# Optimization experiments

Hardware: AMD Instinct MI355X
Metric: run time of the kernel (lower is better)

The kernel has to match this reference:

```python
import jax, jax.numpy as jnp
import numpy as np

N = 50000      # nodes
E = 800000     # edges (avg degree 16)
IN = 128       # in_feats
OUT = 128      # out_feats
H = 8          # num_heads
D = OUT // H   # out_heads (per-head dim) = 16


def _xavier(key, shape, fan_in, fan_out):
    bound = np.sqrt(6.0 / (fan_in + fan_out)).astype(np.float32)
    return jax.random.uniform(key, shape, jnp.float32, -bound, bound)


def setup_inputs() -> dict:
    key = jax.random.key(0)
    ks = jax.random.split(key, 12)
    feat = jax.random.normal(ks[0], (N, IN), jnp.float32)
    src = jax.random.randint(ks[1], (E,), 0, N, jnp.int32)
    dst = jax.random.randint(ks[2], (E,), 0, N, jnp.int32)
    # stacked per-head Linear weights: nn.Linear(IN, D) per head -> [H, IN, D]
    Wq = _xavier(ks[3], (H, IN, D), IN, D)
    Wk = _xavier(ks[4], (H, IN, D), IN, D)
    Wv = _xavier(ks[5], (H, IN, D), IN, D)
    b = 1.0 / np.sqrt(IN).astype(np.float32)
    bq = jax.random.uniform(ks[6], (H, D), jnp.float32, -b, b)
    bk = jax.random.uniform(ks[7], (H, D), jnp.float32, -b, b)
    bv = jax.random.uniform(ks[8], (H, D), jnp.float32, -b, b)
    # residual self projection W_self: Linear(IN, OUT), stored as [IN, OUT]
    Ws = _xavier(ks[9], (IN, OUT), IN, OUT)
    bs = jax.random.uniform(ks[10], (OUT,), jnp.float32, -b, b)
    return {"feat": feat, "src": src, "dst": dst,
            "Wq": Wq, "bq": bq, "Wk": Wk, "bk": bk, "Wv": Wv, "bv": bv,
            "Ws": Ws, "bs": bs}


def reference(feat, src, dst, Wq, bq, Wk, bk, Wv, bv, Ws, bs):
    # per-head projections, all heads at once: [N, H, D]
    q = jnp.einsum('ni,hid->nhd', feat, Wq) + bq
    k = jnp.einsum('ni,hid->nhd', feat, Wk) + bk
    v = jnp.einsum('ni,hid->nhd', feat, Wv) + bv

    # edge scores: sum_d k[src] * q[dst], scaled by sqrt(D)  -> [E, H]
    scores = jnp.einsum('ehd,ehd->eh', k[src], q[dst]) / np.sqrt(D).astype(np.float32)

    # edge_softmax: segment softmax over incoming edges of each dst node
    m = jax.ops.segment_max(scores, dst, num_segments=N)          # [N, H]
    m = jax.lax.stop_gradient(jnp.where(jnp.isfinite(m), m, 0.0))
    ex = jnp.exp(scores - m[dst])                                  # [E, H]
    den = jax.ops.segment_sum(ex, dst, num_segments=N)            # [N, H]
    attn = ex / den[dst]                                           # [E, H]

    # weighted scatter-sum aggregation: h[dst] += attn * v[src]
    msg = v[src] * attn[:, :, None]                                # [E, H, D]
    h = jax.ops.segment_sum(msg, dst, num_segments=N)              # [N, H, D]

    rst = h.reshape(N, H * D)
    # residual: W_self(feat_dst)
    rst = rst + feat @ Ws + bs
    return rst
```

## Files before the change

kernel.cpp:

```cpp
#include <hip/hip_runtime.h>
#include <hip/hip_bf16.h>

typedef unsigned short u16;
typedef unsigned int u32;
typedef __attribute__((ext_vector_type(4))) unsigned int uint4v;
typedef __bf16 bf16x8 __attribute__((ext_vector_type(8)));
typedef float f32x4 __attribute__((ext_vector_type(4)));

#define INF 128
#define OUTF 128
#define NHEAD 8
#define HDIM 16
#define CAP 48
#define NBUCK 196
#define BSHIFT 8
#define BNODES 256
#define BCAP 4608
#define ECHUNK 4096

#if __has_builtin(__builtin_amdgcn_global_load_lds)
#define HAS_GLL 1
#else
#define HAS_GLL 0
#endif

__device__ __forceinline__ float lo2f(u32 u) { return __uint_as_float(u << 16); }
__device__ __forceinline__ float hi2f(u32 u) { return __uint_as_float(u & 0xffff0000u); }
__device__ __forceinline__ float bf2f(u16 b) { return __uint_as_float(((u32)b) << 16); }
__device__ __forceinline__ u16 f2bf(float x) {
    __hip_bfloat16 h = __float2bfloat16(x);
    return *reinterpret_cast<u16*>(&h);
}
__device__ __forceinline__ float fast_exp2(float x) {
    return __builtin_amdgcn_exp2f(x);
}

__device__ __forceinline__ void load8(const void* base, size_t eoff, int isf32, float o[8]) {
    if (isf32) {
        const float* p = (const float*)base + eoff;
        float4 a = *(const float4*)p;
        float4 b = *(const float4*)(p + 4);
        o[0] = a.x; o[1] = a.y; o[2] = a.z; o[3] = a.w;
        o[4] = b.x; o[5] = b.y; o[6] = b.z; o[7] = b.w;
    } else {
        uint4v u = *(const uint4v*)((const u16*)base + eoff);
        o[0] = lo2f(u.x); o[1] = hi2f(u.x);
        o[2] = lo2f(u.y); o[3] = hi2f(u.y);
        o[4] = lo2f(u.z); o[5] = hi2f(u.z);
        o[6] = lo2f(u.w); o[7] = hi2f(u.w);
    }
}

__device__ __forceinline__ uint4v pack8(const float v[8]) {
    uint4v u;
    u.x = (u32)f2bf(v[0]) | ((u32)f2bf(v[1]) << 16);
    u.y = (u32)f2bf(v[2]) | ((u32)f2bf(v[3]) << 16);
    u.z = (u32)f2bf(v[4]) | ((u32)f2bf(v[5]) << 16);
    u.w = (u32)f2bf(v[6]) | ((u32)f2bf(v[7]) << 16);
    return u;
}

__device__ __forceinline__ f32x4 mfma16(bf16x8 a, bf16x8 b, f32x4 c) {
    return __builtin_amdgcn_mfma_f32_16x16x32_bf16(a, b, c, 0, 0, 0);
}

__global__ __launch_bounds__(256) void prep_kernel(
    const u32* __restrict__ featw,
    const void* __restrict__ Wq, const void* __restrict__ bq,
    const void* __restrict__ Wk, const void* __restrict__ bk,
    const void* __restrict__ Wv, const void* __restrict__ bv,
    const void* __restrict__ Ws, const void* __restrict__ bs,
    u16* __restrict__ Wcat, float* __restrict__ bcat, int* __restrict__ flag,
    int* __restrict__ bucketCursor)
{
    __shared__ int sflag;
    const int tid = threadIdx.x;
    if (tid < 64) {
        float mx = 0.f;
#pragma unroll
        for (int i = 0; i < 4; ++i) {
            u32 u = featw[tid * 4 + i];
            float a = fabsf(lo2f(u));
            float b = fabsf(hi2f(u));
            if (!(a < 1e30f)) a = 1e30f;
            if (!(b < 1e30f)) b = 1e30f;
            mx = fmaxf(mx, fmaxf(a, b));
        }
#pragma unroll
        for (int off = 32; off; off >>= 1) mx = fmaxf(mx, __shfl_xor(mx, off));
        if (tid == 0) sflag = (mx > 1e6f) ? 1 : 0;
    }
    __syncthreads();
    const int isf32 = sflag;
    if (blockIdx.x == 0 && tid == 0) *flag = isf32;

    const int wi = blockIdx.x * 256 + tid;
    if (wi < NBUCK) bucketCursor[wi] = 0;

    const int col = wi >> 4, ch = wi & 15;
    const int mat = col >> 7, c = col & 127;
    const void* W = (mat == 0) ? Wq : (mat == 1) ? Wk : (mat == 2) ? Wv : Ws;
    const void* bb = (mat == 0) ? bq : (mat == 1) ? bk : (mat == 2) ? bv : bs;
    size_t base; int stride;
    if (mat < 3) { int h = c >> 4, d = c & 15; base = (size_t)h * (INF * HDIM) + d; stride = HDIM; }
    else { base = c; stride = OUTF; }
#pragma unroll
    for (int j = 0; j < 8; ++j) {
        int i = ch * 8 + j;
        float w = isf32 ? ((const float*)W)[base + (size_t)i * stride]
                        : bf2f(((const u16*)W)[base + (size_t)i * stride]);
        Wcat[(size_t)col * INF + i] = f2bf(w);
    }
    if (ch == 0) bcat[col] = isf32 ? ((const float*)bb)[c] : bf2f(((const u16*)bb)[c]);
}

__global__ __launch_bounds__(256) void fused_kernel(
    const void* __restrict__ feat, const u16* __restrict__ Wcat,
    const float* __restrict__ bcat,
    u16* __restrict__ qb, u16* __restrict__ kb, u16* __restrict__ vb,
    void* __restrict__ outp, const int* __restrict__ flag, int N,
    const int* __restrict__ dst, const int* __restrict__ srcv,
    int* __restrict__ bucketCursor, u32* __restrict__ bucketArr,
    int E, int projBlocks)
{
    __shared__ __attribute__((aligned(16))) char ldsraw[16384];
    const int tid = threadIdx.x;

    if (blockIdx.x >= projBlocks) {
        int* hist  = (int*)ldsraw;
        int* gbase = hist + NBUCK;
        int* hist2 = gbase + NBUCK;
        const int e0 = (blockIdx.x - projBlocks) * ECHUNK;
        for (int i = tid; i < NBUCK; i += 256) { hist[i] = 0; hist2[i] = 0; }
        __syncthreads();
#pragma unroll
        for (int i = 0; i < 16; ++i) {
            int e = e0 + i * 256 + tid;
            if (e < E) atomicAdd(&hist[dst[e] >> BSHIFT], 1);
        }
        __syncthreads();
        for (int i = tid; i < NBUCK; i += 256)
            gbase[i] = atomicAdd(&bucketCursor[i], hist[i]);
        __syncthreads();
#pragma unroll
        for (int i = 0; i < 16; ++i) {
            int e = e0 + i * 256 + tid;
            if (e < E) {
                int d = dst[e], s = srcv[e];
                int b = d >> BSHIFT;
                int loc = atomicAdd(&hist2[b], 1);
                int idx = gbase[b] + loc;
                if (idx < BCAP)
                    bucketArr[(size_t)b * BCAP + idx] =
                        ((u32)(d & (BNODES - 1)) << 16) | (u32)s;
            }
        }
        return;
    }

    const int isf32 = *flag;
    char* sb = ldsraw;
    const int n0 = blockIdx.x * 64;
    const int w = tid >> 6, l = tid & 63;

#if HAS_GLL
    if (!isf32) {
        const char* fb = (const char*)feat;
#pragma unroll
        for (int i = 0; i < 4; ++i) {
            int p = w * 4096 + i * 1024 + l * 16;
            int row = p >> 8, pk = p & 255;
            int rowg = n0 + row; if (rowg >= N) rowg = N - 1;
            const char* gsrc = fb + (size_t)rowg * 256 + (pk ^ ((row & 7) << 4));
            __builtin_amdgcn_global_load_lds(
                (const __attribute__((address_space(1))) void*)gsrc,
                (__attribute__((address_space(3))) void*)(sb + w * 4096 + i * 1024),
                16, 0, 0);
        }
    } else
#endif
    {
        int row = tid >> 2;
        int k0 = (tid & 3) * 32;
        int rowg = n0 + row; if (rowg >= N) rowg = N - 1;
        size_t goff = (size_t)rowg * INF + k0;
#pragma unroll
        for (int m = 0; m < 4; ++m) {
            float t[8];
            load8(feat, goff + m * 8, isf32, t);
            uint4v pk = pack8(t);
            int kbyte = 2 * (k0 + m * 8);
            int off = row * 256 + (kbyte ^ ((row & 7) << 4));
            *(uint4v*)(sb + off) = pk;
        }
    }
    __syncthreads();

    const int lrow = l & 15, lk = l >> 4;
    const int j = lrow;

    const u16* wb = Wcat + (size_t)(w * 128 + lrow) * INF + lk * 8;
    u32* bp = (w == 0) ? (u32*)qb : (w == 1) ? (u32*)kb
             : (w == 2) ? (u32*)vb : (u32*)outp;
    const int src16 = (j & 7) * 2;

#pragma unroll
    for (int rth = 0; rth < 2; ++rth) {
        bf16x8 af[2][4];
#pragma unroll
        for (int rt = 0; rt < 2; ++rt) {
            int row = (rth * 2 + rt) * 16 + lrow;
#pragma unroll
            for (int ks = 0; ks < 4; ++ks) {
                int kbyte = ks * 64 + lk * 16;
                int off = row * 256 + (kbyte ^ ((row & 7) << 4));
                af[rt][ks] = *(const bf16x8*)(sb + off);
            }
        }

#pragma unroll
        for (int ctp = 0; ctp < 4; ++ctp) {
            const int ctA = 2 * ctp, ctB = 2 * ctp + 1;
            bf16x8 bA[4], bB[4];
#pragma unroll
            for (int ks = 0; ks < 4; ++ks) {
                bA[ks] = *(const bf16x8*)(wb + (size_t)ctA * 16 * INF + ks * 32);
                bB[ks] = *(const bf16x8*)(wb + (size_t)ctB * 16 * INF + ks * 32);
            }
            f32x4 accA[2] = {{0,0,0,0},{0,0,0,0}};
            f32x4 accB[2] = {{0,0,0,0},{0,0,0,0}};
#pragma unroll
            for (int ks = 0; ks < 4; ++ks)
#pragma unroll
                for (int rt = 0; rt < 2; ++rt) {
                    accA[rt] = mfma16(af[rt][ks], bA[ks], accA[rt]);
                    accB[rt] = mfma16(af[rt][ks], bB[ks], accB[rt]);
                }

            float biasA = bcat[w * 128 + ctA * 16 + lrow];
            float biasB = bcat[w * 128 + ctB * 16 + lrow];
#pragma unroll
            for (int rt = 0; rt < 2; ++rt) {
#pragma unroll
                for (int r = 0; r < 4; ++r) {
                    int node = n0 + (rth * 2 + rt) * 16 + lk * 4 + r;
                    float vA = accA[rt][r] + biasA;
                    float vB = accB[rt][r] + biasB;
                    if (w == 3 && isf32) {
                        if (node < N) {
                            ((float*)outp)[(size_t)node * OUTF + ctA * 16 + lrow] = vA;
                            ((float*)outp)[(size_t)node * OUTF + ctB * 16 + lrow] = vB;
                        }
                    } else {
                        float pvA = __shfl_xor(vA, 1);
                        float pvB = __shfl_xor(vB, 1);
                        u32 pkA = (u32)f2bf(vA) | ((u32)f2bf(pvA) << 16);
                        u32 pkB = (u32)f2bf(vB) | ((u32)f2bf(pvB) << 16);
                        u32 a = __shfl(pkA, src16, 16);
                        u32 b = __shfl(pkB, src16, 16);
                        u32 val = (j & 8) ? b : a;
                        if (node < N) bp[(size_t)node * 64 + ctp * 16 + j] = val;
                    }
                }
            }
        }
    }
}

__global__ __launch_bounds__(256) void csr_kernel(
    const u32* __restrict__ bucketArr, const int* __restrict__ bucketCursor,
    int* __restrict__ cursor, u16* __restrict__ srcs16, int N)
{
    __shared__ int cnt[BNODES];
    __shared__ u16 seg[BNODES * CAP];
    const int b = blockIdx.x;
    const int tid = threadIdx.x;
    const int nodeBase = b << BSHIFT;

    for (int i = tid; i < BNODES; i += 256) cnt[i] = 0;
    __syncthreads();

    int m = bucketCursor[b]; if (m > BCAP) m = BCAP;
    const u32* ap = bucketArr + (size_t)b * BCAP;
    for (int i = tid; i < m; i += 256) {
        u32 pr = ap[i];
        int dloc = pr >> 16;
        int pos = atomicAdd(&cnt[dloc], 1);
        if (pos < CAP) seg[dloc * CAP + pos] = (u16)(pr & 0xffffu);
    }
    __syncthreads();

    uint4v* so = (uint4v*)(srcs16 + (size_t)nodeBase * CAP);
    const uint4v* si = (const uint4v*)seg;
    const int nvec = BNODES * CAP / 8;
    for (int i = tid; i < nvec; i += 256) so[i] = si[i];
    for (int i = tid; i < BNODES; i += 256) {
        int n = nodeBase + i;
        if (n < N) cursor[n] = cnt[i];
    }
}

__global__ __launch_bounds__(256) void attn_kernel(
    const u16* __restrict__ qb, const u16* __restrict__ kb, const u16* __restrict__ vb,
    const int* __restrict__ cursor, const u16* __restrict__ srcs16,
    void* __restrict__ outp, const int* __restrict__ flag, int N,
    int nodeBase, int nodeCount)
{
    const int n = nodeBase + blockIdx.x * 4 + (threadIdx.x >> 6);
    if (n >= nodeBase + nodeCount || n >= N) return;
    const int isf32 = *flag;
    const int lane = threadIdx.x & 63;

    const u32* __restrict__ kdw = (const u32*)kb;
    const u32* __restrict__ vdw = (const u32*)vb;

    const float C = 0.36067376022224085f;
    const u32 qu = ((const u32*)qb)[(size_t)n * 64 + lane];
    const float q0 = lo2f(qu) * C, q1 = hi2f(qu) * C;

    int cnt = cursor[n]; if (cnt > CAP) cnt = CAP;
    const u16* sp = srcs16 + (size_t)n * CAP;

    float den = 0.f, a0 = 0.f, a1 = 0.f;
    int p = 0;
    for (; p + 8 <= cnt; p += 8) {
        int s[8];
#pragma unroll
        for (int j = 0; j < 8; ++j) s[j] = sp[p + j];
        u32 ku[8], vu[8];
#pragma unroll
        for (int j = 0; j < 8; ++j) {
            ku[j] = kdw[(size_t)s[j] * 64 + lane];
            vu[j] = vdw[(size_t)s[j] * 64 + lane];
        }
        float pr[8];
#pragma unroll
        for (int j = 0; j < 8; ++j) pr[j] = fmaf(hi2f(ku[j]), q1, lo2f(ku[j]) * q0);
#pragma unroll
        for (int off = 1; off < 8; off <<= 1)
#pragma unroll
            for (int j = 0; j < 8; ++j) pr[j] += __shfl_xor(pr[j], off);
#pragma unroll
        for (int j = 0; j < 8; ++j) {
            float e = fast_exp2(pr[j]);
            den += e;
            a0 = fmaf(e, lo2f(vu[j]), a0);
            a1 = fmaf(e, hi2f(vu[j]), a1);
        }
    }
    for (; p < cnt; ++p) {
        int s = sp[p];
        u32 ku = kdw[(size_t)s * 64 + lane];
        u32 vu = vdw[(size_t)s * 64 + lane];
        float pr = fmaf(hi2f(ku), q1, lo2f(ku) * q0);
        pr += __shfl_xor(pr, 1); pr += __shfl_xor(pr, 2); pr += __shfl_xor(pr, 4);
        float e = fast_exp2(pr);
        den += e;
        a0 = fmaf(e, lo2f(vu), a0);
        a1 = fmaf(e, hi2f(vu), a1);
    }
    float inv = (den > 0.f) ? (1.0f / den) : 0.f;
    float r0 = a0 * inv, r1 = a1 * inv;
    if (isf32) {
        float2* op = (float2*)outp + (size_t)n * 64 + lane;
        float2 o = *op; o.x += r0; o.y += r1; *op = o;
    } else {
        u32* op = (u32*)outp + (size_t)n * 64 + lane;
        u32 ou = *op;
        u32 pk = (u32)f2bf(lo2f(ou) + r0) | ((u32)f2bf(hi2f(ou) + r1) << 16);
        *op = pk;
    }
}

extern "C" void kernel_launch(void* const* d_in, const int* in_sizes, int n_in,
                              void* d_out, int out_size, void* d_ws, size_t ws_size,
                              hipStream_t stream) {
    const void* feat = d_in[0];
    const int* src  = (const int*)d_in[1];
    const int* dst  = (const int*)d_in[2];
    const void* Wq = d_in[3]; const void* bq = d_in[4];
    const void* Wk = d_in[5]; const void* bk = d_in[6];
    const void* Wv = d_in[7]; const void* bv = d_in[8];
    const void* Ws = d_in[9]; const void* bs = d_in[10];

    const int N = in_sizes[0] / INF;
    const int E = in_sizes[1];

    u16* qb = (u16*)d_ws;
    u16* kb = qb + (size_t)N * OUTF;
    u16* vb = kb + (size_t)N * OUTF;
    u16* Wcat = vb + (size_t)N * OUTF;
    float* bcat = (float*)(Wcat + 512 * INF);
    int* cursor  = (int*)(bcat + 512);
    int* flag    = cursor + N;
    int* bucketCursor = flag + 1;
    u16* srcs16  = (u16*)(bucketCursor + NBUCK);
    u32* bucketArr = (u32*)(srcs16 + (size_t)NBUCK * BNODES * CAP);

    const int projBlocks = (N + 63) / 64;
    const int partBlocks = (E + ECHUNK - 1) / ECHUNK;

    prep_kernel<<<32, 256, 0, stream>>>((const u32*)feat, Wq, bq, Wk, bk, Wv, bv, Ws, bs,
                                        Wcat, bcat, flag, bucketCursor);
    fused_kernel<<<projBlocks + partBlocks, 256, 0, stream>>>(
        feat, Wcat, bcat, qb, kb, vb, d_out, flag, N,
        dst, src, bucketCursor, bucketArr, E, projBlocks);
    csr_kernel<<<NBUCK, 256, 0, stream>>>(bucketArr, bucketCursor, cursor, srcs16, N);
    const int half = (N + 1) / 2;
    attn_kernel<<<(half + 3) / 4, 256, 0, stream>>>(qb, kb, vb, cursor, srcs16,
                                                    d_out, flag, N, 0, half);
    attn_kernel<<<(N - half + 3) / 4, 256, 0, stream>>>(qb, kb, vb, cursor, srcs16,
                                                        d_out, flag, N, half, N - half);
}
```

Before: 128.7 us.

## Split fused projection/partition kernel and launch attention in four chunks

The combined kernel, which ran projection blocks and edge-partition blocks side by side, becomes two separate kernels, proj_kernel and part_kernel. Each now has its own launch, and the partition kernel uses smaller static LDS. The attention launch is split into four node ranges instead of two. This may reduce divergence and resource contention from mixing heterogeneous blocks, but it adds kernel launches and removes the overlap between projection and partitioning.

```diff
diff --git a/kernel.cpp b/kernel.cpp
--- a/kernel.cpp
+++ b/kernel.cpp
@@ -114,50 +114,14 @@
     if (ch == 0) bcat[col] = isf32 ? ((const float*)bb)[c] : bf2f(((const u16*)bb)[c]);
 }
 
-__global__ __launch_bounds__(256) void fused_kernel(
+__global__ __launch_bounds__(256) void proj_kernel(
     const void* __restrict__ feat, const u16* __restrict__ Wcat,
     const float* __restrict__ bcat,
     u16* __restrict__ qb, u16* __restrict__ kb, u16* __restrict__ vb,
-    void* __restrict__ outp, const int* __restrict__ flag, int N,
-    const int* __restrict__ dst, const int* __restrict__ srcv,
-    int* __restrict__ bucketCursor, u32* __restrict__ bucketArr,
-    int E, int projBlocks)
+    void* __restrict__ outp, const int* __restrict__ flag, int N)
 {
     __shared__ __attribute__((aligned(16))) char ldsraw[16384];
     const int tid = threadIdx.x;
-
-    if (blockIdx.x >= projBlocks) {
-        int* hist  = (int*)ldsraw;
-        int* gbase = hist + NBUCK;
-        int* hist2 = gbase + NBUCK;
-        const int e0 = (blockIdx.x - projBlocks) * ECHUNK;
-        for (int i = tid; i < NBUCK; i += 256) { hist[i] = 0; hist2[i] = 0; }
-        __syncthreads();
-#pragma unroll
-        for (int i = 0; i < 16; ++i) {
-            int e = e0 + i * 256 + tid;
-            if (e < E) atomicAdd(&hist[dst[e] >> BSHIFT], 1);
-        }
-        __syncthreads();
-        for (int i = tid; i < NBUCK; i += 256)
-            gbase[i] = atomicAdd(&bucketCursor[i], hist[i]);
-        __syncthreads();
-#pragma unroll
-        for (int i = 0; i < 16; ++i) {
-            int e = e0 + i * 256 + tid;
-            if (e < E) {
-                int d = dst[e], s = srcv[e];
-                int b = d >> BSHIFT;
-                int loc = atomicAdd(&hist2[b], 1);
-                int idx = gbase[b] + loc;
-                if (idx < BCAP)
-                    bucketArr[(size_t)b * BCAP + idx] =
-                        ((u32)(d & (BNODES - 1)) << 16) | (u32)s;
-            }
-        }
-        return;
-    }
-
     const int isf32 = *flag;
     char* sb = ldsraw;
     const int n0 = blockIdx.x * 64;
@@ -267,6 +231,40 @@
     }
 }
 
+__global__ __launch_bounds__(256) void part_kernel(
+    const int* __restrict__ dst, const int* __restrict__ srcv,
+    int* __restrict__ bucketCursor, u32* __restrict__ bucketArr, int E)
+{
+    __shared__ int hist[NBUCK], gbase[NBUCK], hist2[NBUCK];
+    const int tid = threadIdx.x;
+    const int e0 = blockIdx.x * ECHUNK;
+
+    for (int i = tid; i < NBUCK; i += 256) { hist[i] = 0; hist2[i] = 0; }
+    __syncthreads();
+#pragma unroll
+    for (int i = 0; i < 16; ++i) {
+        int e = e0 + i * 256 + tid;
+        if (e < E) atomicAdd(&hist[dst[e] >> BSHIFT], 1);
+    }
+    __syncthreads();
+    for (int i = tid; i < NBUCK; i += 256)
+        gbase[i] = atomicAdd(&bucketCursor[i], hist[i]);
+    __syncthreads();
+#pragma unroll
+    for (int i = 0; i < 16; ++i) {
+        int e = e0 + i * 256 + tid;
+        if (e < E) {
+            int d = dst[e], s = srcv[e];
+            int b = d >> BSHIFT;
+            int loc = atomicAdd(&hist2[b], 1);
+            int idx = gbase[b] + loc;
+            if (idx < BCAP)
+                bucketArr[(size_t)b * BCAP + idx] =
+                    ((u32)(d & (BNODES - 1)) << 16) | (u32)s;
+        }
+    }
+}
+
 __global__ __launch_bounds__(256) void csr_kernel(
     const u32* __restrict__ bucketArr, const int* __restrict__ bucketCursor,
     int* __restrict__ cursor, u16* __restrict__ srcs16, int N)
@@ -402,13 +400,16 @@
 
     prep_kernel<<<32, 256, 0, stream>>>((const u32*)feat, Wq, bq, Wk, bk, Wv, bv, Ws, bs,
                                         Wcat, bcat, flag, bucketCursor);
-    fused_kernel<<<projBlocks + partBlocks, 256, 0, stream>>>(
-        feat, Wcat, bcat, qb, kb, vb, d_out, flag, N,
-        dst, src, bucketCursor, bucketArr, E, projBlocks);
+    proj_kernel<<<projBlocks, 256, 0, stream>>>(feat, Wcat, bcat, qb, kb, vb,
+                                                d_out, flag, N);
+    part_kernel<<<partBlocks, 256, 0, stream>>>(dst, src, bucketCursor, bucketArr, E);
     csr_kernel<<<NBUCK, 256, 0, stream>>>(bucketArr, bucketCursor, cursor, srcs16, N);
-    const int half = (N + 1) / 2;
-    attn_kernel<<<(half + 3) / 4, 256, 0, stream>>>(qb, kb, vb, cursor, srcs16,
-                                                    d_out, flag, N, 0, half);
-    attn_kernel<<<(N - half + 3) / 4, 256, 0, stream>>>(qb, kb, vb, cursor, srcs16,
-                                                        d_out, flag, N, half, N - half);
-}
+    const int quarter = (N + 3) / 4;
+    for (int qi = 0; qi < 4; ++qi) {
+        int base = qi * quarter;
+        int count = (base + quarter <= N) ? quarter : (N - base);
+        if (count > 0)
+            attn_kernel<<<(count + 3) / 4, 256, 0, stream>>>(
+                qb, kb, vb, cursor, srcs16, d_out, flag, N, base, count);
+    }
+}
```

After: 160.0 us. 1.24x slower.
